# Performance work log

Measured on AMD Instinct MI355X. Metric: run time of the kernel, lower is better.

Reference implementation:

```python
import jax, jax.numpy as jnp
import numpy as np

NUM_CODES = 2048
CODE_DEPTH = 64
D_MODEL = 1024
EMA_DECAY = 0.99


def setup_inputs() -> dict:
    key = jax.random.key(0)
    ks = jax.random.split(key, 4)
    x = jax.random.normal(ks[0], (8, 2048, D_MODEL), dtype=jnp.float32)
    # downsampler Linear(d_model, code_depth)
    W_down = jax.random.normal(ks[1], (CODE_DEPTH, D_MODEL), dtype=jnp.float32) / np.sqrt(D_MODEL)
    b_down = jnp.zeros((CODE_DEPTH,), dtype=jnp.float32)
    # codebook: randn, row-normalized, code 0 zeroed (padding code)
    cb = jax.random.normal(ks[2], (1, NUM_CODES, CODE_DEPTH), dtype=jnp.float32)
    cb = cb / jnp.linalg.norm(cb, axis=-1, keepdims=True)
    cb = cb.at[:, 0].set(0.0)
    cluster_sizes = jnp.zeros((1, NUM_CODES), dtype=jnp.float32)
    cluster_sums = jnp.zeros((1, NUM_CODES, CODE_DEPTH), dtype=jnp.float32)
    return {"x": x, "W_down": W_down, "b_down": b_down, "codebook": cb,
            "cluster_sizes": cluster_sizes, "cluster_sums": cluster_sums}


def reference(x, W_down, b_down, codebook, cluster_sizes, cluster_sums):
    """Quantizer.forward, level=0, training=True, quantize=True, mask=None,
    gumbel=False, reverse_ema=False, ema_decay>0."""
    decay = EMA_DECAY
    num_codes = codebook.shape[1]
    cb = codebook[0]                                   # [K, D]
    # downsample + L2 normalize
    z = jnp.einsum('bsm,dm->bsd', x, W_down) + b_down  # [B, S, D]
    z = z / jnp.linalg.norm(z, axis=-1, keepdims=True)
    zd = jax.lax.stop_gradient(z)
    # cdist(z.detach(), codebook[1:]) -> euclidean distances [B, S, K-1]
    codes = cb[1:]
    d2 = (jnp.sum(zd * zd, -1, keepdims=True)
          + jnp.sum(codes * codes, -1)
          - 2.0 * jnp.einsum('bsd,kd->bsk', zd, codes))
    dist = jnp.sqrt(jnp.maximum(d2, 0.0))
    code_indices = jnp.argmin(dist, axis=-1) + 1       # [B, S], in [1, K)
    hard = cb[code_indices]                            # embedding lookup
    # commitment loss: mse(hard.detach(), z)
    commitment_loss = jnp.mean((jax.lax.stop_gradient(hard) - z) ** 2)
    # one-hot aggregation
    onehot = jax.nn.one_hot(code_indices, num_codes, dtype=z.dtype)  # [B,S,K]
    flat_onehot = onehot.reshape(-1, num_codes)        # [N, K]
    bincounts = flat_onehot.sum(axis=0)                # [K]
    used = bincounts != 0                              # [K] bool
    # unused-code loss: mean of per-(batch,code) min distance over unused codes
    code_dist = jnp.min(dist, axis=-2)                 # [B, K-1]
    unused_mask = ~used[1:]                            # [K-1]
    cnt = jnp.sum(unused_mask.astype(jnp.float32)) * code_dist.shape[0]
    unused_code_loss = jnp.sum(code_dist * unused_mask[None, :]) / jnp.maximum(cnt, 1.0)
    # EMA scatter update (forward/standard EMA)
    obs = zd.reshape(-1, zd.shape[-1])                 # [N, D]
    sums = flat_onehot.T @ obs                         # [K, D]
    new_cs = decay * cluster_sizes[0] + (1.0 - decay) * jax.lax.stop_gradient(bincounts)
    new_csum = decay * cluster_sums[0] + (1.0 - decay) * jax.lax.stop_gradient(sums)
    n = new_cs.sum()
    smoothed = (new_cs + 1e-5) * n / (n + num_codes * 1e-5)
    centroids = new_csum / smoothed[:, None]
    new_cb = jnp.where(used[:, None], jax.lax.stop_gradient(centroids), cb)
    new_cb = new_cb.at[0].set(0.0)
    # straight-through estimator
    hard_codes = z + jax.lax.stop_gradient(hard - z)
    embedding_loss = unused_code_loss
    return (hard_codes, code_indices, commitment_loss, embedding_loss,
            new_cb[None], new_cs[None], new_csum[None])
```

## Files before the change

kernel.cpp:

```cpp
#include <hip/hip_runtime.h>

#define NROWS 16384
#define DM    1024
#define CD    64
#define NC    2048
#define KC    2047
#define NB    8
#define DECAY 0.99f

#define K3_BLOCKS 512

#define OUT_HARD   0
#define OUT_IDX    1048576
#define OUT_COMMIT 1064960
#define OUT_EMB    1064961
#define OUT_CB     1064962
#define OUT_CS     1196034
#define OUT_CSUM   1198082

#define WS_Z      0
#define WS_CN2    1048576
#define WS_BINC   1050624
#define WS_SUMS   1052672
#define WS_CDIST  1183744
#define WS_COMMIT 1200120
#define WS_ZN2    1200632
#define WS_N      1217016
#define WS_PART   1298940
#define WS_BV     WS_PART
#define WS_BI     (WS_PART + 262144)
#define WS_IDXM   (WS_PART + 524288)

#define F32_INF_BITS 0x7F800000u

__global__ __launch_bounds__(256) void k0_init(const float* __restrict__ cb,
                                               float* __restrict__ ws) {
  int i = blockIdx.x * 256 + threadIdx.x;
  if (i < NC * CD) (ws + WS_SUMS)[i] = 0.0f;
  if (i < NC) {
    ((unsigned*)(ws + WS_BINC))[i] = 0u;
    float cn2;
    if (i < KC) {
      const float* c = cb + (size_t)(i + 1) * CD;
      float s0 = 0.f, s1 = 0.f;
      #pragma unroll
      for (int d = 0; d < CD; d += 2) { s0 = fmaf(c[d], c[d], s0); s1 = fmaf(c[d+1], c[d+1], s1); }
      cn2 = s0 + s1;
    } else {
      cn2 = __uint_as_float(F32_INF_BITS);
    }
    (ws + WS_CN2)[i] = cn2;
  }
  if (i < NB * KC) ((unsigned*)(ws + WS_CDIST))[i] = F32_INF_BITS;
}

__global__ __launch_bounds__(128) void k1_split(const float* __restrict__ x,
                                                const float* __restrict__ W,
                                                float* __restrict__ ws) {
  __shared__ float xs[32][132];
  __shared__ float wls[32][68];
  const int t = threadIdx.x;
  const int ks = blockIdx.x & 3;
  const int row0 = (blockIdx.x >> 2) * 128;
  const int kbase = ks * 256;
  const int tx = t & 7, ty = t >> 3;
  const int sseg = t & 7, srow = t >> 3;

  float4 px[8], pw[4];
  auto ld = [&](int kt) {
    const int kk = kbase + kt * 32;
    #pragma unroll
    for (int it = 0; it < 8; ++it)
      px[it] = *(const float4*)(x + (size_t)(row0 + srow + 16 * it) * DM + kk + sseg * 4);
    #pragma unroll
    for (int it = 0; it < 4; ++it)
      pw[it] = *(const float4*)(W + (size_t)(srow + 16 * it) * DM + kk + sseg * 4);
  };
  ld(0);

  float acc[8][8];
  #pragma unroll
  for (int i = 0; i < 8; i++)
    #pragma unroll
    for (int j = 0; j < 8; j++) acc[i][j] = 0.f;

  for (int kt = 0; kt < 8; ++kt) {
    __syncthreads();
    const int sg4 = sseg * 4;
    #pragma unroll
    for (int it = 0; it < 8; ++it) {
      const int cpos = (srow + 16 * it) ^ ((sseg & 3) << 3);
      xs[sg4 + 0][cpos] = px[it].x; xs[sg4 + 1][cpos] = px[it].y;
      xs[sg4 + 2][cpos] = px[it].z; xs[sg4 + 3][cpos] = px[it].w;
    }
    #pragma unroll
    for (int it = 0; it < 4; ++it) {
      const int wcol = srow + 16 * it;
      wls[sg4 + 0][wcol] = pw[it].x; wls[sg4 + 1][wcol] = pw[it].y;
      wls[sg4 + 2][wcol] = pw[it].z; wls[sg4 + 3][wcol] = pw[it].w;
    }
    __syncthreads();
    if (kt < 7) ld(kt + 1);

    #pragma unroll 4
    for (int dl = 0; dl < 32; ++dl) {
      const int xcol = (ty * 8) ^ (((dl >> 2) & 3) << 3);
      float4 xv0 = *(const float4*)(&xs[dl][xcol]);
      float4 xv1 = *(const float4*)(&xs[dl][xcol + 4]);
      float4 wv0 = *(const float4*)(&wls[dl][tx * 8]);
      float4 wv1 = *(const float4*)(&wls[dl][tx * 8 + 4]);
      float xz[8] = {xv0.x, xv0.y, xv0.z, xv0.w, xv1.x, xv1.y, xv1.z, xv1.w};
      float wc[8] = {wv0.x, wv0.y, wv0.z, wv0.w, wv1.x, wv1.y, wv1.z, wv1.w};
      #pragma unroll
      for (int i = 0; i < 8; i++)
        #pragma unroll
        for (int j = 0; j < 8; j++)
          acc[i][j] = fmaf(xz[i], wc[j], acc[i][j]);
    }
  }

  float* part = ws + WS_PART + (size_t)ks * NROWS * CD;
  #pragma unroll
  for (int i = 0; i < 8; i++) {
    const int row = row0 + ty * 8 + i;
    float4 v0, v1;
    v0.x = acc[i][0]; v0.y = acc[i][1]; v0.z = acc[i][2]; v0.w = acc[i][3];
    v1.x = acc[i][4]; v1.y = acc[i][5]; v1.z = acc[i][6]; v1.w = acc[i][7];
    *(float4*)(part + (size_t)row * CD + tx * 8) = v0;
    *(float4*)(part + (size_t)row * CD + tx * 8 + 4) = v1;
  }
}

__global__ __launch_bounds__(256) void k1_reduce(const float* __restrict__ bdown,
                                                 float* __restrict__ ws) {
  const int t = threadIdx.x;
  const int tx = t & 15, ty = t >> 4;
  const int row = blockIdx.x * 16 + ty;
  const float* part = ws + WS_PART;
  const size_t off = (size_t)row * CD + tx * 4;

  float4 v0 = *(const float4*)(part + off);
  float4 v1 = *(const float4*)(part + (size_t)1 * NROWS * CD + off);
  float4 v2 = *(const float4*)(part + (size_t)2 * NROWS * CD + off);
  float4 v3 = *(const float4*)(part + (size_t)3 * NROWS * CD + off);
  float4 b  = *(const float4*)(bdown + tx * 4);
  float4 v;
  v.x = (v0.x + v1.x) + (v2.x + v3.x) + b.x;
  v.y = (v0.y + v1.y) + (v2.y + v3.y) + b.y;
  v.z = (v0.z + v1.z) + (v2.z + v3.z) + b.z;
  v.w = (v0.w + v1.w) + (v2.w + v3.w) + b.w;

  float ss = v.x * v.x + v.y * v.y + v.z * v.z + v.w * v.w;
  #pragma unroll
  for (int m = 1; m < 16; m <<= 1) ss += __shfl_xor(ss, m, 64);
  float inv = 1.0f / sqrtf(ss);
  float4 zv; zv.x = v.x * inv; zv.y = v.y * inv; zv.z = v.z * inv; zv.w = v.w * inv;
  *(float4*)(ws + WS_Z + off) = zv;
  if (tx == 0) (ws + WS_ZN2)[row] = ss * inv * inv;
}

__global__ __launch_bounds__(256) void k1_down(const float* __restrict__ x,
                                               const float* __restrict__ W,
                                               const float* __restrict__ bdown,
                                               float* __restrict__ ws) {
  __shared__ float xs[64][68];
  __shared__ float wls[64][68];
  const int t = threadIdx.x;
  const int row0 = blockIdx.x * 64;
  const int tx = t & 15, ty = t >> 4;

  int pr[4], pseg[4];
  #pragma unroll
  for (int it = 0; it < 4; ++it) { int c = t + it * 256; pr[it] = c >> 4; pseg[it] = c & 15; }

  float4 px[4], pw[4];
  #pragma unroll
  for (int it = 0; it < 4; ++it) {
    px[it] = *(const float4*)(x + (size_t)(row0 + pr[it]) * DM + pseg[it] * 4);
    pw[it] = *(const float4*)(W + (size_t)pr[it] * DM + pseg[it] * 4);
  }

  float acc[4][4];
  #pragma unroll
  for (int i = 0; i < 4; i++)
    #pragma unroll
    for (int j = 0; j < 4; j++) acc[i][j] = 0.f;

  for (int kt = 0; kt < 16; ++kt) {
    __syncthreads();
    #pragma unroll
    for (int it = 0; it < 4; ++it) {
      *(float4*)(&xs[pr[it]][pseg[it] * 4]) = px[it];
      *(float4*)(&wls[pr[it]][pseg[it] * 4]) = pw[it];
    }
    __syncthreads();
    if (kt < 15) {
      const int k0 = (kt + 1) * 64;
      #pragma unroll
      for (int it = 0; it < 4; ++it) {
        px[it] = *(const float4*)(x + (size_t)(row0 + pr[it]) * DM + k0 + pseg[it] * 4);
        pw[it] = *(const float4*)(W + (size_t)pr[it] * DM + k0 + pseg[it] * 4);
      }
    }
    #pragma unroll 4
    for (int k = 0; k < 64; k += 4) {
      float4 xv[4], wv[4];
      #pragma unroll
      for (int i = 0; i < 4; i++) xv[i] = *(const float4*)(&xs[ty * 4 + i][k]);
      #pragma unroll
      for (int j = 0; j < 4; j++) wv[j] = *(const float4*)(&wls[tx * 4 + j][k]);
      #pragma unroll
      for (int i = 0; i < 4; i++)
        #pragma unroll
        for (int j = 0; j < 4; j++)
          acc[i][j] = fmaf(xv[i].x, wv[j].x, fmaf(xv[i].y, wv[j].y,
                      fmaf(xv[i].z, wv[j].z, fmaf(xv[i].w, wv[j].w, acc[i][j]))));
    }
  }

  #pragma unroll
  for (int j = 0; j < 4; j++) {
    float bj = bdown[tx * 4 + j];
    #pragma unroll
    for (int i = 0; i < 4; i++) acc[i][j] += bj;
  }

  float* z = ws + WS_Z;
  float* zn2 = ws + WS_ZN2;
  #pragma unroll
  for (int i = 0; i < 4; i++) {
    float ss = acc[i][0] * acc[i][0] + acc[i][1] * acc[i][1] +
               acc[i][2] * acc[i][2] + acc[i][3] * acc[i][3];
    #pragma unroll
    for (int m = 1; m < 16; m <<= 1) ss += __shfl_xor(ss, m, 64);
    float inv = 1.0f / sqrtf(ss);
    float4 zv;
    zv.x = acc[i][0] * inv; zv.y = acc[i][1] * inv;
    zv.z = acc[i][2] * inv; zv.w = acc[i][3] * inv;
    int row = row0 + ty * 4 + i;
    *(float4*)(z + (size_t)row * CD + tx * 4) = zv;
    if (tx == 0) zn2[row] = ss * inv * inv;
  }
}

__global__ __launch_bounds__(256) void k2_dist(const float* __restrict__ cbp,
                                               float* __restrict__ ws) {
  __shared__ float zT[64][132];
  __shared__ float cT[64][132];
  __shared__ float cn2s[128];
  __shared__ float zn2s[128];
  __shared__ unsigned colmin[128];

  const int t = threadIdx.x;
  const int gq = blockIdx.x & 15;
  const int rt = blockIdx.x >> 4;
  const int row0 = rt << 7;
  const int batch = rt >> 4;
  const int tx = t & 15, ty = t >> 4;
  const float* z = ws + WS_Z;
  unsigned* cdist = (unsigned*)(ws + WS_CDIST) + (size_t)batch * KC;

  if (t < 128) {
    zn2s[t] = (ws + WS_ZN2)[row0 + t];
    cn2s[t] = (ws + WS_CN2)[gq * 128 + t];
    colmin[t] = F32_INF_BITS;
  }

  const int sr = t & 127;
  const int sodd = t >> 7;
  const int ccol = sr ^ (((sr >> 5) & 3) << 2);
  const int gc = gq * 128 + sr;
  float4 pzv[8], pcv[8];
  #pragma unroll
  for (int it = 0; it < 8; ++it) {
    const int seg = 2 * it + sodd;
    pzv[it] = *(const float4*)(z + (size_t)(row0 + sr) * CD + seg * 4);
    pcv[it] = (gc < KC) ? *(const float4*)(cbp + (size_t)(gc + 1) * CD + seg * 4)
                        : make_float4(0.f, 0.f, 0.f, 0.f);
  }
  #pragma unroll
  for (int it = 0; it < 8; ++it) {
    const int sg4 = (2 * it + sodd) * 4;
    zT[sg4 + 0][sr] = pzv[it].x; zT[sg4 + 1][sr] = pzv[it].y;
    zT[sg4 + 2][sr] = pzv[it].z; zT[sg4 + 3][sr] = pzv[it].w;
    cT[sg4 + 0][ccol] = pcv[it].x; cT[sg4 + 1][ccol] = pcv[it].y;
    cT[sg4 + 2][ccol] = pcv[it].z; cT[sg4 + 3][ccol] = pcv[it].w;
  }
  __syncthreads();

  float acc[8][8];
  #pragma unroll
  for (int i = 0; i < 8; i++)
    #pragma unroll
    for (int j = 0; j < 8; j++) acc[i][j] = 0.f;

  const int col0 = (tx * 8) ^ (((tx >> 2) & 3) << 2);
  const int col1 = (tx * 8 + 4) ^ (((tx >> 2) & 3) << 2);
  #pragma unroll 8
  for (int d = 0; d < 64; ++d) {
    float4 za = *(const float4*)(&zT[d][ty * 8]);
    float4 zb = *(const float4*)(&zT[d][ty * 8 + 4]);
    float4 ca = *(const float4*)(&cT[d][col0]);
    float4 cb2 = *(const float4*)(&cT[d][col1]);
    float zz[8] = {za.x, za.y, za.z, za.w, zb.x, zb.y, zb.z, zb.w};
    float cc[8] = {ca.x, ca.y, ca.z, ca.w, cb2.x, cb2.y, cb2.z, cb2.w};
    #pragma unroll
    for (int i = 0; i < 8; i++)
      #pragma unroll
      for (int j = 0; j < 8; j++)
        acc[i][j] = fmaf(zz[i], cc[j], acc[i][j]);
  }

  float bestv[8];
  int besti[8];
  #pragma unroll
  for (int i = 0; i < 8; i++) { bestv[i] = __uint_as_float(F32_INF_BITS); besti[i] = 0; }

  #pragma unroll
  for (int jl = 0; jl < 8; ++jl) {
    const int jloc = tx * 8 + jl;
    const int jg = gq * 128 + jloc;
    const float c2 = cn2s[jloc];
    float colv = __uint_as_float(F32_INF_BITS);
    #pragma unroll
    for (int i = 0; i < 8; ++i) {
      float s = fmaf(-2.f, acc[i][jl], c2);
      if (s < bestv[i]) { bestv[i] = s; besti[i] = jg; }
      float v = zn2s[ty * 8 + i] + s;
      v = v < 0.f ? 0.f : v;
      colv = v < colv ? v : colv;
    }
    colv = fminf(colv, __shfl_xor(colv, 16, 64));
    colv = fminf(colv, __shfl_xor(colv, 32, 64));
    if ((t & 48) == 0) atomicMin(&colmin[jloc], __float_as_uint(colv));
  }

  #pragma unroll
  for (int m = 1; m <= 8; m <<= 1) {
    #pragma unroll
    for (int i = 0; i < 8; i++) {
      float ov = __shfl_xor(bestv[i], m, 64);
      int oi = __shfl_xor(besti[i], m, 64);
      if (ov < bestv[i] || (ov == bestv[i] && oi < besti[i])) { bestv[i] = ov; besti[i] = oi; }
    }
  }
  if (tx == 0) {
    #pragma unroll
    for (int i = 0; i < 8; i++) {
      const int row = row0 + ty * 8 + i;
      (ws + WS_BV)[(size_t)gq * NROWS + row] = bestv[i];
      ((int*)(ws + WS_BI))[(size_t)gq * NROWS + row] = besti[i] + 1;
    }
  }

  __syncthreads();
  if (t < 128) {
    const int jg2 = gq * 128 + t;
    if (jg2 < KC) atomicMin(&cdist[jg2], colmin[t]);
  }
}

__global__ __launch_bounds__(256) void k2b_merge(float* __restrict__ ws,
                                                 float* __restrict__ out) {
  const int row = blockIdx.x * 256 + threadIdx.x;
  float bv = (ws + WS_BV)[row];
  int bi = ((const int*)(ws + WS_BI))[row];
  #pragma unroll
  for (int g2 = 1; g2 < 16; ++g2) {
    float v = (ws + WS_BV)[(size_t)g2 * NROWS + row];
    int i2 = ((const int*)(ws + WS_BI))[(size_t)g2 * NROWS + row];
    if (v < bv) { bv = v; bi = i2; }
  }
  ((int*)(ws + WS_IDXM))[row] = bi;
  out[OUT_IDX + row] = (float)bi;
}

__global__ __launch_bounds__(256) void k3_scatter(const float* __restrict__ cb,
                                                  float* __restrict__ ws,
                                                  float* __restrict__ out) {
  const int t = threadIdx.x;
  const int lane = t & 63;
  const int w = t >> 6;
  const int rowbase = blockIdx.x * 32 + w * 8;
  const float* z = ws + WS_Z;
  const int* idxp = (const int*)(ws + WS_IDXM);

  int idx[8];
  #pragma unroll
  for (int r = 0; r < 8; ++r) idx[r] = idxp[rowbase + r];

  float sq = 0.f;
  #pragma unroll
  for (int r = 0; r < 8; ++r) {
    const int row = rowbase + r;
    const float c = cb[(size_t)idx[r] * CD + lane];
    const float zv = z[(size_t)row * CD + lane];
    out[OUT_HARD + (size_t)row * CD + lane] = zv + (c - zv);
    const float d = c - zv;
    sq = fmaf(d, d, sq);
    atomicAdd(ws + WS_SUMS + (size_t)idx[r] * CD + lane, zv);
    if (lane == 0) atomicAdd((unsigned*)(ws + WS_BINC) + idx[r], 1u);
  }

  __shared__ float red[4];
  #pragma unroll
  for (int m = 1; m < 64; m <<= 1) sq += __shfl_xor(sq, m, 64);
  if (lane == 0) red[w] = sq;
  __syncthreads();
  if (t == 0) (ws + WS_COMMIT)[blockIdx.x] = red[0] + red[1] + red[2] + red[3];
}

__global__ __launch_bounds__(1024) void k4a_stats(const float* __restrict__ cs_in,
                                                  float* __restrict__ ws,
                                                  float* __restrict__ out) {
  __shared__ float red[1024];
  const int t = threadIdx.x;
  const unsigned* binc = (const unsigned*)(ws + WS_BINC);

  float npart = 0.f;
  #pragma unroll
  for (int i = t; i < NC; i += 1024) {
    float nc = DECAY * cs_in[i] + (1.f - DECAY) * (float)binc[i];
    out[OUT_CS + i] = nc;
    npart += nc;
  }
  red[t] = npart; __syncthreads();
  for (int s = 512; s > 0; s >>= 1) { if (t < s) red[t] += red[t + s]; __syncthreads(); }
  if (t == 0) (ws + WS_N)[0] = red[0];
  __syncthreads();

  float cpart = 0.f;
  for (int j = t; j < K3_BLOCKS; j += 1024) cpart += (ws + WS_COMMIT)[j];
  red[t] = cpart; __syncthreads();
  for (int s = 512; s > 0; s >>= 1) { if (t < s) red[t] += red[t + s]; __syncthreads(); }
  float commit = red[0]; __syncthreads();

  const unsigned* cdist = (const unsigned*)(ws + WS_CDIST);
  float lsum = 0.f, ccount = 0.f;
  for (int j = t; j < KC; j += 1024) {
    if (binc[j + 1] == 0u) {
      ccount += 1.f;
      float srow = 0.f;
      #pragma unroll
      for (int b = 0; b < NB; b++) srow += sqrtf(__uint_as_float(cdist[b * KC + j]));
      lsum += srow;
    }
  }
  red[t] = lsum; __syncthreads();
  for (int s = 512; s > 0; s >>= 1) { if (t < s) red[t] += red[t + s]; __syncthreads(); }
  float totloss = red[0]; __syncthreads();
  red[t] = ccount; __syncthreads();
  for (int s = 512; s > 0; s >>= 1) { if (t < s) red[t] += red[t + s]; __syncthreads(); }
  float cnt = red[0] * (float)NB;
  if (t == 0) {
    out[OUT_COMMIT] = commit / (float)(NROWS * CD);
    out[OUT_EMB] = totloss / fmaxf(cnt, 1.f);
  }
}

__global__ __launch_bounds__(256) void k4b_update(const float* __restrict__ cb,
                                                  const float* __restrict__ csum_in,
                                                  const float* __restrict__ ws,
                                                  float* __restrict__ out) {
  const int e = blockIdx.x * 256 + threadIdx.x;
  const int k = e >> 6;
  const unsigned* binc = (const unsigned*)(ws + WS_BINC);
  const float n = (ws + WS_N)[0];
  const float denom = n + (float)NC * 1e-5f;

  float ncsum = DECAY * csum_in[e] + (1.f - DECAY) * (ws + WS_SUMS)[e];
  out[OUT_CSUM + e] = ncsum;
  float smoothed = (out[OUT_CS + k] + 1e-5f) * n / denom;
  float cent = ncsum / smoothed;
  float v = (binc[k] != 0u) ? cent : cb[e];
  if (k == 0) v = 0.f;
  out[OUT_CB + e] = v;
}

extern "C" void kernel_launch(void* const* d_in, const int* in_sizes, int n_in,
                              void* d_out, int out_size, void* d_ws, size_t ws_size,
                              hipStream_t stream) {
  const float* x    = (const float*)d_in[0];
  const float* W    = (const float*)d_in[1];
  const float* b    = (const float*)d_in[2];
  const float* cb   = (const float*)d_in[3];
  const float* cs   = (const float*)d_in[4];
  const float* csum = (const float*)d_in[5];
  float* out = (float*)d_out;
  float* ws  = (float*)d_ws;

  const size_t need = ((size_t)WS_PART + (size_t)4 * NROWS * CD) * sizeof(float);
  const bool use_split = ws_size >= need;

  hipLaunchKernelGGL(k0_init, dim3(512), dim3(256), 0, stream, cb, ws);
  if (use_split) {
    hipLaunchKernelGGL(k1_split,  dim3(512),  dim3(128), 0, stream, x, W, ws);
    hipLaunchKernelGGL(k1_reduce, dim3(1024), dim3(256), 0, stream, b, ws);
  } else {
    hipLaunchKernelGGL(k1_down, dim3(256), dim3(256), 0, stream, x, W, b, ws);
  }
  hipLaunchKernelGGL(k2_dist,   dim3(2048),      dim3(256),  0, stream, cb, ws);
  hipLaunchKernelGGL(k2b_merge, dim3(64),        dim3(256),  0, stream, ws, out);
  hipLaunchKernelGGL(k3_scatter,dim3(K3_BLOCKS), dim3(256),  0, stream, cb, ws, out);
  hipLaunchKernelGGL(k4a_stats, dim3(1),         dim3(1024), 0, stream, cs, ws, out);
  hipLaunchKernelGGL(k4b_update,dim3(512),       dim3(256),  0, stream, cb, csum, ws, out);
}
```

Measured before the change: 155.4 us.

## Loop each distance block over four codebook tiles, reusing the z tile

The distance kernel now uses 512-thread blocks that load a 128-row z tile once and loop over four 128-code codebook tiles. The next codebook tile is prefetched into registers during compute. This cuts redundant z reloads, shrinks the partial argmin buffers from 16 groups to 4, and makes the merge kernel cheaper. In exchange each block is serialised with extra barriers, the grid shrinks to 512 blocks, and each thread holds half as many accumulators, which lowers arithmetic intensity per LDS read.

```diff
diff --git a/kernel.cpp b/kernel.cpp
--- a/kernel.cpp
+++ b/kernel.cpp
@@ -28,8 +28,8 @@
 #define WS_N      1217016
 #define WS_PART   1298940
 #define WS_BV     WS_PART
-#define WS_BI     (WS_PART + 262144)
-#define WS_IDXM   (WS_PART + 524288)
+#define WS_BI     (WS_PART + 65536)
+#define WS_IDXM   (WS_PART + 131072)
 
 #define F32_INF_BITS 0x7F800000u
 
@@ -243,7 +243,7 @@
   }
 }
 
-__global__ __launch_bounds__(256) void k2_dist(const float* __restrict__ cbp,
+__global__ __launch_bounds__(512) void k2_dist(const float* __restrict__ cbp,
                                                float* __restrict__ ws) {
   __shared__ float zT[64][132];
   __shared__ float cT[64][132];
@@ -252,91 +252,112 @@
   __shared__ unsigned colmin[128];
 
   const int t = threadIdx.x;
-  const int gq = blockIdx.x & 15;
-  const int rt = blockIdx.x >> 4;
+  const int gq = blockIdx.x & 3;
+  const int rt = blockIdx.x >> 2;
   const int row0 = rt << 7;
   const int batch = rt >> 4;
-  const int tx = t & 15, ty = t >> 4;
+  const int tx = t & 31, ty = t >> 5;
   const float* z = ws + WS_Z;
+  const float* cn2p = ws + WS_CN2;
   unsigned* cdist = (unsigned*)(ws + WS_CDIST) + (size_t)batch * KC;
 
-  if (t < 128) {
-    zn2s[t] = (ws + WS_ZN2)[row0 + t];
-    cn2s[t] = (ws + WS_CN2)[gq * 128 + t];
-    colmin[t] = F32_INF_BITS;
-  }
-
-  const int sr = t & 127;
-  const int sodd = t >> 7;
-  const int ccol = sr ^ (((sr >> 5) & 3) << 2);
-  const int gc = gq * 128 + sr;
-  float4 pzv[8], pcv[8];
-  #pragma unroll
-  for (int it = 0; it < 8; ++it) {
-    const int seg = 2 * it + sodd;
-    pzv[it] = *(const float4*)(z + (size_t)(row0 + sr) * CD + seg * 4);
-    pcv[it] = (gc < KC) ? *(const float4*)(cbp + (size_t)(gc + 1) * CD + seg * 4)
-                        : make_float4(0.f, 0.f, 0.f, 0.f);
-  }
-  #pragma unroll
-  for (int it = 0; it < 8; ++it) {
-    const int sg4 = (2 * it + sodd) * 4;
-    zT[sg4 + 0][sr] = pzv[it].x; zT[sg4 + 1][sr] = pzv[it].y;
-    zT[sg4 + 2][sr] = pzv[it].z; zT[sg4 + 3][sr] = pzv[it].w;
-    cT[sg4 + 0][ccol] = pcv[it].x; cT[sg4 + 1][ccol] = pcv[it].y;
-    cT[sg4 + 2][ccol] = pcv[it].z; cT[sg4 + 3][ccol] = pcv[it].w;
-  }
-  __syncthreads();
-
-  float acc[8][8];
-  #pragma unroll
-  for (int i = 0; i < 8; i++)
-    #pragma unroll
-    for (int j = 0; j < 8; j++) acc[i][j] = 0.f;
-
-  const int col0 = (tx * 8) ^ (((tx >> 2) & 3) << 2);
-  const int col1 = (tx * 8 + 4) ^ (((tx >> 2) & 3) << 2);
-  #pragma unroll 8
-  for (int d = 0; d < 64; ++d) {
-    float4 za = *(const float4*)(&zT[d][ty * 8]);
-    float4 zb = *(const float4*)(&zT[d][ty * 8 + 4]);
-    float4 ca = *(const float4*)(&cT[d][col0]);
-    float4 cb2 = *(const float4*)(&cT[d][col1]);
-    float zz[8] = {za.x, za.y, za.z, za.w, zb.x, zb.y, zb.z, zb.w};
-    float cc[8] = {ca.x, ca.y, ca.z, ca.w, cb2.x, cb2.y, cb2.z, cb2.w};
-    #pragma unroll
-    for (int i = 0; i < 8; i++)
-      #pragma unroll
-      for (int j = 0; j < 8; j++)
-        acc[i][j] = fmaf(zz[i], cc[j], acc[i][j]);
-  }
+  if (t < 128) zn2s[t] = (ws + WS_ZN2)[row0 + t];
+
+  {
+    const int sr = t >> 2, sp = t & 3;
+    float4 v[4];
+    #pragma unroll
+    for (int it = 0; it < 4; ++it)
+      v[it] = *(const float4*)(z + (size_t)(row0 + sr) * CD + (sp + 4 * it) * 4);
+    #pragma unroll
+    for (int it = 0; it < 4; ++it) {
+      const int sg4 = (sp + 4 * it) * 4;
+      zT[sg4 + 0][sr] = v[it].x; zT[sg4 + 1][sr] = v[it].y;
+      zT[sg4 + 2][sr] = v[it].z; zT[sg4 + 3][sr] = v[it].w;
+    }
+  }
+
+  const int cr = t >> 2, cp = t & 3;
+  const int ccol = cr ^ (((cr >> 5) & 3) << 2);
+  float4 pc[4];
+  auto ldc = [&](int lt) {
+    const int code = gq * 512 + lt * 128 + cr;
+    #pragma unroll
+    for (int it = 0; it < 4; ++it)
+      pc[it] = (code < KC) ? *(const float4*)(cbp + (size_t)(code + 1) * CD + (cp + 4 * it) * 4)
+                           : make_float4(0.f, 0.f, 0.f, 0.f);
+  };
+  ldc(0);
 
   float bestv[8];
   int besti[8];
   #pragma unroll
   for (int i = 0; i < 8; i++) { bestv[i] = __uint_as_float(F32_INF_BITS); besti[i] = 0; }
 
-  #pragma unroll
-  for (int jl = 0; jl < 8; ++jl) {
-    const int jloc = tx * 8 + jl;
-    const int jg = gq * 128 + jloc;
-    const float c2 = cn2s[jloc];
-    float colv = __uint_as_float(F32_INF_BITS);
-    #pragma unroll
-    for (int i = 0; i < 8; ++i) {
-      float s = fmaf(-2.f, acc[i][jl], c2);
-      if (s < bestv[i]) { bestv[i] = s; besti[i] = jg; }
-      float v = zn2s[ty * 8 + i] + s;
-      v = v < 0.f ? 0.f : v;
-      colv = v < colv ? v : colv;
-    }
-    colv = fminf(colv, __shfl_xor(colv, 16, 64));
-    colv = fminf(colv, __shfl_xor(colv, 32, 64));
-    if ((t & 48) == 0) atomicMin(&colmin[jloc], __float_as_uint(colv));
-  }
-
-  #pragma unroll
-  for (int m = 1; m <= 8; m <<= 1) {
+  const int ccol0 = (tx * 4) ^ (((tx >> 3) & 3) << 2);
+
+  for (int lt = 0; lt < 4; ++lt) {
+    __syncthreads();
+    #pragma unroll
+    for (int it = 0; it < 4; ++it) {
+      const int sg4 = (cp + 4 * it) * 4;
+      cT[sg4 + 0][ccol] = pc[it].x; cT[sg4 + 1][ccol] = pc[it].y;
+      cT[sg4 + 2][ccol] = pc[it].z; cT[sg4 + 3][ccol] = pc[it].w;
+    }
+    if (t < 128) {
+      cn2s[t] = cn2p[gq * 512 + lt * 128 + t];
+      colmin[t] = F32_INF_BITS;
+    }
+    __syncthreads();
+    if (lt < 3) ldc(lt + 1);
+
+    float acc[8][4];
+    #pragma unroll
+    for (int i = 0; i < 8; i++)
+      #pragma unroll
+      for (int j = 0; j < 4; j++) acc[i][j] = 0.f;
+
+    #pragma unroll 8
+    for (int d = 0; d < 64; ++d) {
+      float4 za = *(const float4*)(&zT[d][ty * 8]);
+      float4 zb = *(const float4*)(&zT[d][ty * 8 + 4]);
+      float4 cv = *(const float4*)(&cT[d][ccol0]);
+      float zz[8] = {za.x, za.y, za.z, za.w, zb.x, zb.y, zb.z, zb.w};
+      float cc[4] = {cv.x, cv.y, cv.z, cv.w};
+      #pragma unroll
+      for (int i = 0; i < 8; i++)
+        #pragma unroll
+        for (int j = 0; j < 4; j++)
+          acc[i][j] = fmaf(zz[i], cc[j], acc[i][j]);
+    }
+
+    const int jbase = gq * 512 + lt * 128;
+    #pragma unroll
+    for (int jl = 0; jl < 4; ++jl) {
+      const int jloc = tx * 4 + jl;
+      const int jg = jbase + jloc;
+      const float c2 = cn2s[jloc];
+      float colv = __uint_as_float(F32_INF_BITS);
+      #pragma unroll
+      for (int i = 0; i < 8; ++i) {
+        float s = fmaf(-2.f, acc[i][jl], c2);
+        if (s < bestv[i]) { bestv[i] = s; besti[i] = jg; }
+        float v = zn2s[ty * 8 + i] + s;
+        v = v < 0.f ? 0.f : v;
+        colv = v < colv ? v : colv;
+      }
+      colv = fminf(colv, __shfl_xor(colv, 32, 64));
+      if ((t & 32) == 0) atomicMin(&colmin[jloc], __float_as_uint(colv));
+    }
+    __syncthreads();
+    if (t < 128) {
+      const int jg2 = jbase + t;
+      if (jg2 < KC) atomicMin(&cdist[jg2], colmin[t]);
+    }
+  }
+
+  #pragma unroll
+  for (int m = 1; m <= 16; m <<= 1) {
     #pragma unroll
     for (int i = 0; i < 8; i++) {
       float ov = __shfl_xor(bestv[i], m, 64);
@@ -351,12 +372,6 @@
       (ws + WS_BV)[(size_t)gq * NROWS + row] = bestv[i];
       ((int*)(ws + WS_BI))[(size_t)gq * NROWS + row] = besti[i] + 1;
     }
-  }
-
-  __syncthreads();
-  if (t < 128) {
-    const int jg2 = gq * 128 + t;
-    if (jg2 < KC) atomicMin(&cdist[jg2], colmin[t]);
   }
 }
 
@@ -366,7 +381,7 @@
   float bv = (ws + WS_BV)[row];
   int bi = ((const int*)(ws + WS_BI))[row];
   #pragma unroll
-  for (int g2 = 1; g2 < 16; ++g2) {
+  for (int g2 = 1; g2 < 4; ++g2) {
     float v = (ws + WS_BV)[(size_t)g2 * NROWS + row];
     int i2 = ((const int*)(ws + WS_BI))[(size_t)g2 * NROWS + row];
     if (v < bv) { bv = v; bi = i2; }
@@ -499,7 +514,7 @@
   } else {
     hipLaunchKernelGGL(k1_down, dim3(256), dim3(256), 0, stream, x, W, b, ws);
   }
-  hipLaunchKernelGGL(k2_dist,   dim3(2048),      dim3(256),  0, stream, cb, ws);
+  hipLaunchKernelGGL(k2_dist,   dim3(512),       dim3(512),  0, stream, cb, ws);
   hipLaunchKernelGGL(k2b_merge, dim3(64),        dim3(256),  0, stream, ws, out);
   hipLaunchKernelGGL(k3_scatter,dim3(K3_BLOCKS), dim3(256),  0, stream, cb, ws, out);
   hipLaunchKernelGGL(k4a_stats, dim3(1),         dim3(1024), 0, stream, cs, ws, out);
```

New measurement: 139.9 us. -10.0%, faster.
